# Kernel tuning notes

Hardware: AMD Instinct MI355X
Metric: run time of the kernel (lower is better)

## Reference

```python
import jax, jax.numpy as jnp
import numpy as np

H = 8  # num_heads

def setup_inputs() -> dict:
    key = jax.random.key(0)
    ks = jax.random.split(key, 8)
    N, B, E = 1024, 8, 256
    value = jax.random.normal(ks[0], (N, B, E), dtype=jnp.float32)
    pos = jax.random.normal(ks[1], (B * H, N, N), dtype=jnp.float32)
    s = 1.0 / np.sqrt(E)
    in_proj_w = jax.random.uniform(ks[2], (3 * E, E), jnp.float32, -s, s)   # content attn qkv proj
    in_proj_b = jnp.zeros((3 * E,), jnp.float32)
    out_w = jax.random.uniform(ks[3], (E, E), jnp.float32, -s, s)
    out_b = jnp.zeros((E,), jnp.float32)
    return {"value": value, "position_attention_weights": pos,
            "in_proj_w": in_proj_w, "in_proj_b": in_proj_b,
            "out_w": out_w, "out_b": out_b}

def reference(value, position_attention_weights, in_proj_w, in_proj_b, out_w, out_b):
    # value: (N, B, E) seq-first, position_attention_weights: (B*H, N, N)
    N, B, E = value.shape
    Dh = E // H
    qkv = value @ in_proj_w.T + in_proj_b            # (N, B, 3E)
    q, k, v = jnp.split(qkv, 3, axis=-1)
    # (N, B, E) -> (B*H, N, Dh)
    def to_heads(t):
        return t.reshape(N, B * H, Dh).transpose(1, 0, 2)
    q, k, v = to_heads(q), to_heads(k), to_heads(v)
    scale = 1.0 / jnp.sqrt(jnp.asarray(Dh, q.dtype))
    content = jnp.einsum('bnd,bmd->bnm', q * scale, k)   # (B*H, N, N) content scores
    # merge_attention == 'gate': clamp both, log-sigmoid gate on positional, add
    content = jnp.clip(content, -10.0, 10.0)
    pos = jnp.clip(position_attention_weights, -10.0, 10.0)
    scores = jax.nn.log_sigmoid(pos) + content
    attn = jax.nn.softmax(scores, axis=-1)               # normalizer
    out = jnp.einsum('bnm,bmd->bnd', attn, v)            # (B*H, N, Dh)
    out = out.transpose(1, 0, 2).reshape(N, B, E)        # back to (N, B, E)
    out = out @ out_w.T + out_b
    attn_avg = attn.reshape(B, H, N, N).mean(axis=1)     # averaged attention weights
    return out, attn_avg
```

## Files before the change

### kernel.cpp

```cpp
#include <hip/hip_runtime.h>
#include <hip/hip_bf16.h>

typedef __attribute__((ext_vector_type(8))) short short8;
typedef __attribute__((ext_vector_type(4))) float f32x4;
typedef __attribute__((ext_vector_type(4))) unsigned short u16x4;

#define MFMA16(a,b,c) __builtin_amdgcn_mfma_f32_16x16x32_bf16((a),(b),(c),0,0,0)

__device__ __forceinline__ ushort f2bf(float x) {
  union { float f; unsigned u; } v; v.f = x;
  unsigned u = v.u;
  u = (u + 0x7fffu + ((u >> 16) & 1u)) >> 16;
  return (ushort)u;
}

__device__ __forceinline__ float bf2f(ushort u) {
  union { unsigned u; float f; } v; v.u = ((unsigned)u) << 16;
  return v.f;
}

__device__ __forceinline__ short8 ld8(const ushort* p) {
  return *reinterpret_cast<const short8*>(p);
}

__global__ void conv_kernel(const float* __restrict__ value,
                            const float* __restrict__ w_in,
                            const float* __restrict__ w_out,
                            ushort* __restrict__ vbf,
                            ushort* __restrict__ wbf,
                            ushort* __restrict__ owbf) {
  int i = blockIdx.x * 256 + threadIdx.x;
  const float* src; ushort* dst; int j;
  if (i < 524288)      { src = value; dst = vbf;  j = i; }
  else if (i < 573440) { src = w_in;  dst = wbf;  j = i - 524288; }
  else                 { src = w_out; dst = owbf; j = i - 573440; }
  float4 v = reinterpret_cast<const float4*>(src)[j];
  u16x4 o;
  o[0] = f2bf(v.x); o[1] = f2bf(v.y); o[2] = f2bf(v.z); o[3] = f2bf(v.w);
  reinterpret_cast<u16x4*>(dst)[j] = o;
}

__global__ __launch_bounds__(256) void qkv_kernel(
    const ushort* __restrict__ vbf, const ushort* __restrict__ wbf,
    const float* __restrict__ bias,
    ushort* __restrict__ qh, ushort* __restrict__ kh, ushort* __restrict__ vv) {
  int tid = threadIdx.x;
  int wave = tid >> 6, lane = tid & 63;
  int lq = lane & 15, lg = lane >> 4;
  int r0 = blockIdx.x * 16;
  int c0 = (blockIdx.y * 4 + wave) * 16;
  f32x4 acc = {0.f, 0.f, 0.f, 0.f};
  const ushort* ap = vbf + (size_t)(r0 + lq) * 256 + lg * 8;
  const ushort* bp = wbf + (size_t)(c0 + lq) * 256 + lg * 8;
#pragma unroll
  for (int k0 = 0; k0 < 256; k0 += 32)
    acc = MFMA16(ld8(ap + k0), ld8(bp + k0), acc);
  int c = c0 + lq;
  float bv = bias[c];
#pragma unroll
  for (int r = 0; r < 4; ++r) {
    int row = r0 + lg * 4 + r;
    int n = row >> 3, b = row & 7;
    float v = acc[r] + bv;
    if (c < 256) {
      int h = c >> 5, d = c & 31;
      qh[((size_t)(b * 8 + h) * 1024 + n) * 32 + d] = f2bf(v * 0.17677669529663689f);
    } else if (c < 512) {
      int cc = c - 256, h = cc >> 5, d = cc & 31;
      kh[((size_t)(b * 8 + h) * 1024 + n) * 32 + d] = f2bf(v);
    } else {
      int cc = c - 512, h = cc >> 5, d = cc & 31;
      vv[((size_t)(b * 8 + h) * 1024 + n) * 32 + d] = f2bf(v);
    }
  }
}

__global__ __launch_bounds__(256) void vtrans_kernel(const ushort* __restrict__ vv,
                                                     ushort* __restrict__ vt) {
  __shared__ ushort t[32][73];
  int tid = threadIdx.x;
  int bh = blockIdx.y, m0 = blockIdx.x * 64;
  int mm = tid >> 2, d0 = (tid & 3) * 8;
  short8 v = ld8(vv + ((size_t)bh * 1024 + m0 + mm) * 32 + d0);
#pragma unroll
  for (int j = 0; j < 8; ++j) t[d0 + j][mm] = (ushort)v[j];
  __syncthreads();
  int d = tid >> 3, mg = (tid & 7) * 8;
  short8 o;
#pragma unroll
  for (int j = 0; j < 8; ++j) o[j] = (short)t[d][mg + j];
  *reinterpret_cast<short8*>(vt + ((size_t)bh * 32 + d) * 1024 + m0 + mg) = o;
}

__global__ __launch_bounds__(512, 4) void attn_kernel(
    const ushort* __restrict__ qh, const ushort* __restrict__ kh,
    const ushort* __restrict__ vt, const float* __restrict__ pos,
    ushort* __restrict__ ao, float* __restrict__ avg_out) {
  __shared__ __align__(16) ushort attn_lds[16][1028];
  __shared__ float pvred[8][16][32];
  __shared__ float rowsumT[16][8];

  int tid = threadIdx.x;
  int wave = tid >> 6, lane = tid & 63;
  int lq = lane & 15, lg = lane >> 4;
  int n0 = blockIdx.x * 16;
  int b = blockIdx.y;
  int mb = wave * 128;

  float avg[8][4];
#pragma unroll
  for (int t = 0; t < 8; ++t)
#pragma unroll
    for (int r = 0; r < 4; ++r) avg[t][r] = 0.f;

  for (int h = 0; h < 8; ++h) {
    int bh = b * 8 + h;
    short8 qa = ld8(qh + ((size_t)bh * 1024 + n0 + lq) * 32 + lg * 8);
    const ushort* kp = kh + (size_t)bh * 32768 + lg * 8;
    const float* pp = pos + ((size_t)bh << 20);
    float rs[4] = {0.f, 0.f, 0.f, 0.f};
    short8 wreg[4];

    {
      f32x4 S[4];
#pragma unroll
      for (int t = 0; t < 4; ++t) {
        f32x4 z = {0.f, 0.f, 0.f, 0.f};
        S[t] = MFMA16(qa, ld8(kp + (size_t)(mb + lq * 8 + t) * 32), z);
      }
#pragma unroll
      for (int r = 0; r < 4; ++r) {
        int n = n0 + lg * 4 + r;
        float4 p0 = *reinterpret_cast<const float4*>(pp + (size_t)n * 1024 + mb + lq * 8);
        float pv[4] = {p0.x, p0.y, p0.z, p0.w};
#pragma unroll
        for (int t = 0; t < 4; ++t) {
          float p = fminf(10.f, fmaxf(-10.f, pv[t]));
          float c = fminf(10.f, fmaxf(-10.f, S[t][r]));
          float w = __expf(c - 10.f) * __builtin_amdgcn_rcpf(1.f + __expf(-p));
          rs[r] += w;
          wreg[r][t] = (short)f2bf(w);
        }
      }
    }
    {
      f32x4 S[4];
#pragma unroll
      for (int t = 0; t < 4; ++t) {
        f32x4 z = {0.f, 0.f, 0.f, 0.f};
        S[t] = MFMA16(qa, ld8(kp + (size_t)(mb + lq * 8 + 4 + t) * 32), z);
      }
#pragma unroll
      for (int r = 0; r < 4; ++r) {
        int n = n0 + lg * 4 + r;
        float4 p1 = *reinterpret_cast<const float4*>(pp + (size_t)n * 1024 + mb + lq * 8 + 4);
        float pv[4] = {p1.x, p1.y, p1.z, p1.w};
#pragma unroll
        for (int t = 0; t < 4; ++t) {
          float p = fminf(10.f, fmaxf(-10.f, pv[t]));
          float c = fminf(10.f, fmaxf(-10.f, S[t][r]));
          float w = __expf(c - 10.f) * __builtin_amdgcn_rcpf(1.f + __expf(-p));
          rs[r] += w;
          wreg[r][4 + t] = (short)f2bf(w);
        }
      }
    }
#pragma unroll
    for (int r = 0; r < 4; ++r) {
      int row = lg * 4 + r;
      int col = (mb + lq * 8) ^ ((row & 7) << 3);
      *reinterpret_cast<short8*>(&attn_lds[row][col]) = wreg[r];
    }
#pragma unroll
    for (int r = 0; r < 4; ++r) {
      rs[r] += __shfl_xor(rs[r], 1);
      rs[r] += __shfl_xor(rs[r], 2);
      rs[r] += __shfl_xor(rs[r], 4);
      rs[r] += __shfl_xor(rs[r], 8);
    }
    if (lq == 0) {
#pragma unroll
      for (int r = 0; r < 4; ++r) rowsumT[lg * 4 + r][wave] = rs[r];
    }
    f32x4 acc0 = {0.f, 0.f, 0.f, 0.f}, acc1 = {0.f, 0.f, 0.f, 0.f};
    const ushort* vp = vt + (size_t)bh * 32768 + mb + lg * 8;
#pragma unroll
    for (int ks = 0; ks < 4; ++ks) {
      int col = (mb + ks * 32 + lg * 8) ^ ((lq & 7) << 3);
      short8 pa = *reinterpret_cast<const short8*>(&attn_lds[lq][col]);
      acc0 = MFMA16(pa, ld8(vp + (size_t)lq * 1024 + ks * 32), acc0);
      acc1 = MFMA16(pa, ld8(vp + (size_t)(lq + 16) * 1024 + ks * 32), acc1);
    }
    __syncthreads();
    float inv[4];
#pragma unroll
    for (int r = 0; r < 4; ++r) {
      int row = lg * 4 + r;
      float4 a0 = *reinterpret_cast<const float4*>(&rowsumT[row][0]);
      float4 a1 = *reinterpret_cast<const float4*>(&rowsumT[row][4]);
      inv[r] = __builtin_amdgcn_rcpf(a0.x + a0.y + a0.z + a0.w +
                                     a1.x + a1.y + a1.z + a1.w);
    }
#pragma unroll
    for (int r = 0; r < 4; ++r) {
      int row = lg * 4 + r;
      pvred[wave][row][lq] = acc0[r] * inv[r];
      pvred[wave][row][lq + 16] = acc1[r] * inv[r];
    }
#pragma unroll
    for (int r = 0; r < 4; ++r)
#pragma unroll
      for (int t = 0; t < 8; ++t)
        avg[t][r] += bf2f((ushort)wreg[r][t]) * inv[r];
    __syncthreads();
    {
      int n = tid >> 5, d = tid & 31;
      float s = 0.f;
#pragma unroll
      for (int w = 0; w < 8; ++w) s += pvred[w][n][d];
      ao[((size_t)(n0 + n) * 8 + b) * 256 + h * 32 + d] = f2bf(s);
    }
  }
#pragma unroll
  for (int r = 0; r < 4; ++r) {
    int n = n0 + lg * 4 + r;
    float* op = avg_out + (size_t)b * 1048576 + (size_t)n * 1024 + mb + lq * 8;
    float4 v0 = {avg[0][r] * 0.125f, avg[1][r] * 0.125f, avg[2][r] * 0.125f, avg[3][r] * 0.125f};
    float4 v1 = {avg[4][r] * 0.125f, avg[5][r] * 0.125f, avg[6][r] * 0.125f, avg[7][r] * 0.125f};
    *reinterpret_cast<float4*>(op) = v0;
    *reinterpret_cast<float4*>(op + 4) = v1;
  }
}

__global__ __launch_bounds__(256) void oproj_kernel(
    const ushort* __restrict__ ao, const ushort* __restrict__ owbf,
    const float* __restrict__ ob, float* __restrict__ outp) {
  int tid = threadIdx.x;
  int wave = tid >> 6, lane = tid & 63;
  int lq = lane & 15, lg = lane >> 4;
  int r0 = blockIdx.x * 16;
  int c0 = (blockIdx.y * 4 + wave) * 16;
  f32x4 acc = {0.f, 0.f, 0.f, 0.f};
  const ushort* ap = ao + (size_t)(r0 + lq) * 256 + lg * 8;
  const ushort* bp = owbf + (size_t)(c0 + lq) * 256 + lg * 8;
#pragma unroll
  for (int k0 = 0; k0 < 256; k0 += 32)
    acc = MFMA16(ld8(ap + k0), ld8(bp + k0), acc);
  int c = c0 + lq;
  float bv = ob[c];
#pragma unroll
  for (int r = 0; r < 4; ++r) {
    int row = r0 + lg * 4 + r;
    outp[(size_t)row * 256 + c] = acc[r] + bv;
  }
}

extern "C" void kernel_launch(void* const* d_in, const int* in_sizes, int n_in,
                              void* d_out, int out_size, void* d_ws, size_t ws_size,
                              hipStream_t stream) {
  const float* value = (const float*)d_in[0];
  const float* pos   = (const float*)d_in[1];
  const float* w_in  = (const float*)d_in[2];
  const float* b_in  = (const float*)d_in[3];
  const float* w_out = (const float*)d_in[4];
  const float* b_out = (const float*)d_in[5];

  char* ws = (char*)d_ws;
  ushort* vbf  = (ushort*)(ws);
  ushort* wbf  = (ushort*)(ws + 4194304);
  ushort* owbf = (ushort*)(ws + 4587520);
  ushort* qh   = (ushort*)(ws + 4718592);
  ushort* kh   = (ushort*)(ws + 8912896);
  ushort* vv   = (ushort*)(ws + 13107200);
  ushort* vt   = (ushort*)(ws);
  ushort* ao   = (ushort*)(ws + 17301504);

  float* outp = (float*)d_out;
  float* avgp = outp + 2097152;

  conv_kernel<<<2304, 256, 0, stream>>>(value, w_in, w_out, vbf, wbf, owbf);
  qkv_kernel<<<dim3(512, 12), 256, 0, stream>>>(vbf, wbf, b_in, qh, kh, vv);
  vtrans_kernel<<<dim3(16, 64), 256, 0, stream>>>(vv, vt);
  attn_kernel<<<dim3(64, 8), 512, 0, stream>>>(qh, kh, vt, pos, ao, avgp);
  oproj_kernel<<<dim3(512, 4), 256, 0, stream>>>(ao, owbf, b_out, outp);
}
```

Baseline: 181.8 us.

## Prefetch next head's positional tile, double-buffer reductions, drop one barrier per head

Loads the positional-weight tile for the next head during the current head's PV MFMAs and issues K loads early. The pvred and rowsum shared buffers are double-buffered so one of the two __syncthreads per head can go. Softmax normalisation moves into the post-barrier reduction. Non-temporal loads and stores are used for the streamed pos input and the averaged-attention output. This aims to hide HBM latency on the large pos stream, which dominates this memory-bound kernel, at the cost of more registers under launch_bounds(512,4).

```diff
diff --git a/kernel.cpp b/kernel.cpp
--- a/kernel.cpp
+++ b/kernel.cpp
@@ -21,6 +21,14 @@
 
 __device__ __forceinline__ short8 ld8(const ushort* p) {
   return *reinterpret_cast<const short8*>(p);
+}
+
+__device__ __forceinline__ f32x4 ldnt4(const float* p) {
+  return __builtin_nontemporal_load(reinterpret_cast<const f32x4*>(p));
+}
+
+__device__ __forceinline__ void stnt4(float* p, f32x4 v) {
+  __builtin_nontemporal_store(v, reinterpret_cast<f32x4*>(p));
 }
 
 __global__ void conv_kernel(const float* __restrict__ value,
@@ -97,8 +105,8 @@
     const ushort* __restrict__ vt, const float* __restrict__ pos,
     ushort* __restrict__ ao, float* __restrict__ avg_out) {
   __shared__ __align__(16) ushort attn_lds[16][1028];
-  __shared__ float pvred[8][16][32];
-  __shared__ float rowsumT[16][8];
+  __shared__ __align__(16) float pvred[2][8][16][32];
+  __shared__ __align__(16) float rowsumT[2][16][8];
 
   int tid = threadIdx.x;
   int wave = tid >> 6, lane = tid & 63;
@@ -113,29 +121,42 @@
 #pragma unroll
     for (int r = 0; r < 4; ++r) avg[t][r] = 0.f;
 
+  const float* prow0 = pos + ((size_t)(b * 8) << 20) + (size_t)(n0 + lg * 4) * 1024 + mb + lq * 8;
+
+  f32x4 pA[4];
+#pragma unroll
+  for (int r = 0; r < 4; ++r) pA[r] = ldnt4(prow0 + (size_t)r * 1024);
+
+  int buf = 0;
   for (int h = 0; h < 8; ++h) {
     int bh = b * 8 + h;
+    const float* prow = prow0 + ((size_t)h << 20);
+    const ushort* kp = kh + (size_t)bh * 32768 + lg * 8;
+
     short8 qa = ld8(qh + ((size_t)bh * 1024 + n0 + lq) * 32 + lg * 8);
-    const ushort* kp = kh + (size_t)bh * 32768 + lg * 8;
-    const float* pp = pos + ((size_t)bh << 20);
+    short8 ka0 = ld8(kp + (size_t)(mb + lq * 8 + 0) * 32);
+    short8 ka1 = ld8(kp + (size_t)(mb + lq * 8 + 1) * 32);
+    short8 ka2 = ld8(kp + (size_t)(mb + lq * 8 + 2) * 32);
+    short8 ka3 = ld8(kp + (size_t)(mb + lq * 8 + 3) * 32);
+    f32x4 pB[4];
+#pragma unroll
+    for (int r = 0; r < 4; ++r) pB[r] = ldnt4(prow + (size_t)r * 1024 + 4);
+
     float rs[4] = {0.f, 0.f, 0.f, 0.f};
     short8 wreg[4];
 
     {
-      f32x4 S[4];
-#pragma unroll
-      for (int t = 0; t < 4; ++t) {
-        f32x4 z = {0.f, 0.f, 0.f, 0.f};
-        S[t] = MFMA16(qa, ld8(kp + (size_t)(mb + lq * 8 + t) * 32), z);
-      }
+      f32x4 z = {0.f, 0.f, 0.f, 0.f};
+      f32x4 S0 = MFMA16(qa, ka0, z);
+      f32x4 S1 = MFMA16(qa, ka1, z);
+      f32x4 S2 = MFMA16(qa, ka2, z);
+      f32x4 S3 = MFMA16(qa, ka3, z);
+      f32x4 S[4] = {S0, S1, S2, S3};
 #pragma unroll
       for (int r = 0; r < 4; ++r) {
-        int n = n0 + lg * 4 + r;
-        float4 p0 = *reinterpret_cast<const float4*>(pp + (size_t)n * 1024 + mb + lq * 8);
-        float pv[4] = {p0.x, p0.y, p0.z, p0.w};
 #pragma unroll
         for (int t = 0; t < 4; ++t) {
-          float p = fminf(10.f, fmaxf(-10.f, pv[t]));
+          float p = fminf(10.f, fmaxf(-10.f, pA[r][t]));
           float c = fminf(10.f, fmaxf(-10.f, S[t][r]));
           float w = __expf(c - 10.f) * __builtin_amdgcn_rcpf(1.f + __expf(-p));
           rs[r] += w;
@@ -144,20 +165,21 @@
       }
     }
     {
-      f32x4 S[4];
-#pragma unroll
-      for (int t = 0; t < 4; ++t) {
-        f32x4 z = {0.f, 0.f, 0.f, 0.f};
-        S[t] = MFMA16(qa, ld8(kp + (size_t)(mb + lq * 8 + 4 + t) * 32), z);
-      }
+      short8 kb0 = ld8(kp + (size_t)(mb + lq * 8 + 4) * 32);
+      short8 kb1 = ld8(kp + (size_t)(mb + lq * 8 + 5) * 32);
+      short8 kb2 = ld8(kp + (size_t)(mb + lq * 8 + 6) * 32);
+      short8 kb3 = ld8(kp + (size_t)(mb + lq * 8 + 7) * 32);
+      f32x4 z = {0.f, 0.f, 0.f, 0.f};
+      f32x4 S0 = MFMA16(qa, kb0, z);
+      f32x4 S1 = MFMA16(qa, kb1, z);
+      f32x4 S2 = MFMA16(qa, kb2, z);
+      f32x4 S3 = MFMA16(qa, kb3, z);
+      f32x4 S[4] = {S0, S1, S2, S3};
 #pragma unroll
       for (int r = 0; r < 4; ++r) {
-        int n = n0 + lg * 4 + r;
-        float4 p1 = *reinterpret_cast<const float4*>(pp + (size_t)n * 1024 + mb + lq * 8 + 4);
-        float pv[4] = {p1.x, p1.y, p1.z, p1.w};
 #pragma unroll
         for (int t = 0; t < 4; ++t) {
-          float p = fminf(10.f, fmaxf(-10.f, pv[t]));
+          float p = fminf(10.f, fmaxf(-10.f, pB[r][t]));
           float c = fminf(10.f, fmaxf(-10.f, S[t][r]));
           float w = __expf(c - 10.f) * __builtin_amdgcn_rcpf(1.f + __expf(-p));
           rs[r] += w;
@@ -180,7 +202,7 @@
     }
     if (lq == 0) {
 #pragma unroll
-      for (int r = 0; r < 4; ++r) rowsumT[lg * 4 + r][wave] = rs[r];
+      for (int r = 0; r < 4; ++r) rowsumT[buf][lg * 4 + r][wave] = rs[r];
     }
     f32x4 acc0 = {0.f, 0.f, 0.f, 0.f}, acc1 = {0.f, 0.f, 0.f, 0.f};
     const ushort* vp = vt + (size_t)bh * 32768 + mb + lg * 8;
@@ -191,44 +213,49 @@
       acc0 = MFMA16(pa, ld8(vp + (size_t)lq * 1024 + ks * 32), acc0);
       acc1 = MFMA16(pa, ld8(vp + (size_t)(lq + 16) * 1024 + ks * 32), acc1);
     }
-    __syncthreads();
-    float inv[4];
+    if (h < 7) {
+      const float* pn = prow + (1u << 20);
+#pragma unroll
+      for (int r = 0; r < 4; ++r) pA[r] = ldnt4(pn + (size_t)r * 1024);
+    }
 #pragma unroll
     for (int r = 0; r < 4; ++r) {
-      int row = lg * 4 + r;
-      float4 a0 = *reinterpret_cast<const float4*>(&rowsumT[row][0]);
-      float4 a1 = *reinterpret_cast<const float4*>(&rowsumT[row][4]);
-      inv[r] = __builtin_amdgcn_rcpf(a0.x + a0.y + a0.z + a0.w +
-                                     a1.x + a1.y + a1.z + a1.w);
-    }
-#pragma unroll
-    for (int r = 0; r < 4; ++r) {
-      int row = lg * 4 + r;
-      pvred[wave][row][lq] = acc0[r] * inv[r];
-      pvred[wave][row][lq + 16] = acc1[r] * inv[r];
-    }
-#pragma unroll
-    for (int r = 0; r < 4; ++r)
-#pragma unroll
-      for (int t = 0; t < 8; ++t)
-        avg[t][r] += bf2f((ushort)wreg[r][t]) * inv[r];
+      pvred[buf][wave][lg * 4 + r][lq] = acc0[r];
+      pvred[buf][wave][lg * 4 + r][lq + 16] = acc1[r];
+    }
     __syncthreads();
     {
+#pragma unroll
+      for (int r = 0; r < 4; ++r) {
+        int row = lg * 4 + r;
+        float4 a0 = *reinterpret_cast<const float4*>(&rowsumT[buf][row][0]);
+        float4 a1 = *reinterpret_cast<const float4*>(&rowsumT[buf][row][4]);
+        float invr = __builtin_amdgcn_rcpf(a0.x + a0.y + a0.z + a0.w +
+                                           a1.x + a1.y + a1.z + a1.w);
+#pragma unroll
+        for (int t = 0; t < 8; ++t)
+          avg[t][r] += bf2f((ushort)wreg[r][t]) * invr;
+      }
       int n = tid >> 5, d = tid & 31;
+      float4 a0 = *reinterpret_cast<const float4*>(&rowsumT[buf][n][0]);
+      float4 a1 = *reinterpret_cast<const float4*>(&rowsumT[buf][n][4]);
+      float invn = __builtin_amdgcn_rcpf(a0.x + a0.y + a0.z + a0.w +
+                                         a1.x + a1.y + a1.z + a1.w);
       float s = 0.f;
 #pragma unroll
-      for (int w = 0; w < 8; ++w) s += pvred[w][n][d];
-      ao[((size_t)(n0 + n) * 8 + b) * 256 + h * 32 + d] = f2bf(s);
-    }
+      for (int w = 0; w < 8; ++w) s += pvred[buf][w][n][d];
+      ao[((size_t)(n0 + n) * 8 + b) * 256 + h * 32 + d] = f2bf(s * invn);
+    }
+    buf ^= 1;
   }
 #pragma unroll
   for (int r = 0; r < 4; ++r) {
     int n = n0 + lg * 4 + r;
     float* op = avg_out + (size_t)b * 1048576 + (size_t)n * 1024 + mb + lq * 8;
-    float4 v0 = {avg[0][r] * 0.125f, avg[1][r] * 0.125f, avg[2][r] * 0.125f, avg[3][r] * 0.125f};
-    float4 v1 = {avg[4][r] * 0.125f, avg[5][r] * 0.125f, avg[6][r] * 0.125f, avg[7][r] * 0.125f};
-    *reinterpret_cast<float4*>(op) = v0;
-    *reinterpret_cast<float4*>(op + 4) = v1;
+    f32x4 v0 = {avg[0][r] * 0.125f, avg[1][r] * 0.125f, avg[2][r] * 0.125f, avg[3][r] * 0.125f};
+    f32x4 v1 = {avg[4][r] * 0.125f, avg[5][r] * 0.125f, avg[6][r] * 0.125f, avg[7][r] * 0.125f};
+    stnt4(op, v0);
+    stnt4(op + 4, v1);
   }
 }
 
```

After: 213.3 us. 1.17x slower.

## Double-buffer positional scores into LDS via async global_load_lds in attention kernel

Applied to the files above, without the earlier changes.

The positional score tiles are now streamed into a double-buffered LDS array with global_load_lds, prefetching the next half-row chunk while the current one is processed. Each head is split into two halves, each with its own QK, weight and PV steps, and the column mapping per wave changes to suit. Softmax normalisation is deferred to the reduction step, which removes one barrier dependency, and the averaged-attention output uses nontemporal stores. This adds about 66KB of LDS, so launch bounds drop occupancy from 4 to 2 blocks, and there are more barriers per head.

```diff
diff --git a/kernel.cpp b/kernel.cpp
--- a/kernel.cpp
+++ b/kernel.cpp
@@ -21,6 +21,12 @@
 
 __device__ __forceinline__ short8 ld8(const ushort* p) {
   return *reinterpret_cast<const short8*>(p);
+}
+
+__device__ __forceinline__ void glds16(const float* g, float* l) {
+  __builtin_amdgcn_global_load_lds(
+      (const __attribute__((address_space(1))) unsigned int*)g,
+      (__attribute__((address_space(3))) unsigned int*)(void*)l, 16, 0, 0);
 }
 
 __global__ void conv_kernel(const float* __restrict__ value,
@@ -92,12 +98,13 @@
   *reinterpret_cast<short8*>(vt + ((size_t)bh * 32 + d) * 1024 + m0 + mg) = o;
 }
 
-__global__ __launch_bounds__(512, 4) void attn_kernel(
+__global__ __launch_bounds__(512, 2) void attn_kernel(
     const ushort* __restrict__ qh, const ushort* __restrict__ kh,
     const ushort* __restrict__ vt, const float* __restrict__ pos,
     ushort* __restrict__ ao, float* __restrict__ avg_out) {
-  __shared__ __align__(16) ushort attn_lds[16][1028];
-  __shared__ float pvred[8][16][32];
+  __shared__ __align__(16) float pos_lds[2][16][516];
+  __shared__ __align__(16) ushort attn_lds[16][1032];
+  __shared__ __align__(16) float pvred[8][16][32];
   __shared__ float rowsumT[16][8];
 
   int tid = threadIdx.x;
@@ -105,72 +112,77 @@
   int lq = lane & 15, lg = lane >> 4;
   int n0 = blockIdx.x * 16;
   int b = blockIdx.y;
-  int mb = wave * 128;
+
+  auto stage = [&](int s) {
+    int buf = s & 1;
+    const float* gb = pos + ((size_t)(b * 8 + (s >> 1)) << 20)
+                          + (size_t)n0 * 1024 + (s & 1) * 512;
+    int r = wave * 2;
+    glds16(gb + (size_t)r * 1024 +       lane * 4, &pos_lds[buf][r][0]);
+    glds16(gb + (size_t)r * 1024 + 256 + lane * 4, &pos_lds[buf][r][256]);
+    glds16(gb + (size_t)(r + 1) * 1024 +       lane * 4, &pos_lds[buf][r + 1][0]);
+    glds16(gb + (size_t)(r + 1) * 1024 + 256 + lane * 4, &pos_lds[buf][r + 1][256]);
+  };
 
   float avg[8][4];
 #pragma unroll
-  for (int t = 0; t < 8; ++t)
-#pragma unroll
-    for (int r = 0; r < 4; ++r) avg[t][r] = 0.f;
+  for (int j = 0; j < 8; ++j)
+#pragma unroll
+    for (int r = 0; r < 4; ++r) avg[j][r] = 0.f;
+
+  stage(0);
+  stage(1);
+  __syncthreads();
 
   for (int h = 0; h < 8; ++h) {
     int bh = b * 8 + h;
+    const ushort* kp = kh + (size_t)bh * 32768;
+    const ushort* vp = vt + (size_t)bh * 32768;
     short8 qa = ld8(qh + ((size_t)bh * 1024 + n0 + lq) * 32 + lg * 8);
-    const ushort* kp = kh + (size_t)bh * 32768 + lg * 8;
-    const float* pp = pos + ((size_t)bh << 20);
+    f32x4 acc0 = {0.f, 0.f, 0.f, 0.f}, acc1 = {0.f, 0.f, 0.f, 0.f};
     float rs[4] = {0.f, 0.f, 0.f, 0.f};
-    short8 wreg[4];
-
-    {
+    u16x4 wA[4], wB[4];
+
+    auto half_body = [&](int hf, u16x4* wv) {
+      int buf = (h * 2 + hf) & 1;
+      int mwin = hf * 512 + wave * 64;
+      int lcol = wave * 64 + lq * 4;
       f32x4 S[4];
 #pragma unroll
       for (int t = 0; t < 4; ++t) {
         f32x4 z = {0.f, 0.f, 0.f, 0.f};
-        S[t] = MFMA16(qa, ld8(kp + (size_t)(mb + lq * 8 + t) * 32), z);
+        S[t] = MFMA16(qa, ld8(kp + (size_t)(mwin + lq * 4 + t) * 32 + lg * 8), z);
       }
 #pragma unroll
       for (int r = 0; r < 4; ++r) {
-        int n = n0 + lg * 4 + r;
-        float4 p0 = *reinterpret_cast<const float4*>(pp + (size_t)n * 1024 + mb + lq * 8);
-        float pv[4] = {p0.x, p0.y, p0.z, p0.w};
+        int row = lg * 4 + r;
+        f32x4 pv = *reinterpret_cast<const f32x4*>(&pos_lds[buf][row][lcol]);
 #pragma unroll
         for (int t = 0; t < 4; ++t) {
           float p = fminf(10.f, fmaxf(-10.f, pv[t]));
           float c = fminf(10.f, fmaxf(-10.f, S[t][r]));
           float w = __expf(c - 10.f) * __builtin_amdgcn_rcpf(1.f + __expf(-p));
           rs[r] += w;
-          wreg[r][t] = (short)f2bf(w);
+          wv[r][t] = f2bf(w);
         }
+        int col = (mwin + lq * 4) ^ ((row & 7) << 3);
+        *reinterpret_cast<u16x4*>(&attn_lds[row][col]) = wv[r];
       }
-    }
-    {
-      f32x4 S[4];
-#pragma unroll
-      for (int t = 0; t < 4; ++t) {
-        f32x4 z = {0.f, 0.f, 0.f, 0.f};
-        S[t] = MFMA16(qa, ld8(kp + (size_t)(mb + lq * 8 + 4 + t) * 32), z);
+#pragma unroll
+      for (int ks = 0; ks < 2; ++ks) {
+        int sb = mwin + ks * 32;
+        int acol = (sb + lg * 8) ^ ((lq & 7) << 3);
+        short8 pa = *reinterpret_cast<const short8*>(&attn_lds[lq][acol]);
+        acc0 = MFMA16(pa, ld8(vp + (size_t)lq * 1024 + sb + lg * 8), acc0);
+        acc1 = MFMA16(pa, ld8(vp + (size_t)(lq + 16) * 1024 + sb + lg * 8), acc1);
       }
-#pragma unroll
-      for (int r = 0; r < 4; ++r) {
-        int n = n0 + lg * 4 + r;
-        float4 p1 = *reinterpret_cast<const float4*>(pp + (size_t)n * 1024 + mb + lq * 8 + 4);
-        float pv[4] = {p1.x, p1.y, p1.z, p1.w};
-#pragma unroll
-        for (int t = 0; t < 4; ++t) {
-          float p = fminf(10.f, fmaxf(-10.f, pv[t]));
-          float c = fminf(10.f, fmaxf(-10.f, S[t][r]));
-          float w = __expf(c - 10.f) * __builtin_amdgcn_rcpf(1.f + __expf(-p));
-          rs[r] += w;
-          wreg[r][4 + t] = (short)f2bf(w);
-        }
-      }
-    }
-#pragma unroll
-    for (int r = 0; r < 4; ++r) {
-      int row = lg * 4 + r;
-      int col = (mb + lq * 8) ^ ((row & 7) << 3);
-      *reinterpret_cast<short8*>(&attn_lds[row][col]) = wreg[r];
-    }
+    };
+
+    half_body(0, wA);
+    __syncthreads();
+    if (h * 2 + 2 < 16) stage(h * 2 + 2);
+    half_body(1, wB);
+
 #pragma unroll
     for (int r = 0; r < 4; ++r) {
       rs[r] += __shfl_xor(rs[r], 1);
@@ -182,53 +194,45 @@
 #pragma unroll
       for (int r = 0; r < 4; ++r) rowsumT[lg * 4 + r][wave] = rs[r];
     }
-    f32x4 acc0 = {0.f, 0.f, 0.f, 0.f}, acc1 = {0.f, 0.f, 0.f, 0.f};
-    const ushort* vp = vt + (size_t)bh * 32768 + mb + lg * 8;
-#pragma unroll
-    for (int ks = 0; ks < 4; ++ks) {
-      int col = (mb + ks * 32 + lg * 8) ^ ((lq & 7) << 3);
-      short8 pa = *reinterpret_cast<const short8*>(&attn_lds[lq][col]);
-      acc0 = MFMA16(pa, ld8(vp + (size_t)lq * 1024 + ks * 32), acc0);
-      acc1 = MFMA16(pa, ld8(vp + (size_t)(lq + 16) * 1024 + ks * 32), acc1);
+#pragma unroll
+    for (int r = 0; r < 4; ++r) {
+      pvred[wave][lg * 4 + r][lq] = acc0[r];
+      pvred[wave][lg * 4 + r][lq + 16] = acc1[r];
     }
     __syncthreads();
-    float inv[4];
+    if (h * 2 + 3 < 16) stage(h * 2 + 3);
 #pragma unroll
     for (int r = 0; r < 4; ++r) {
       int row = lg * 4 + r;
       float4 a0 = *reinterpret_cast<const float4*>(&rowsumT[row][0]);
       float4 a1 = *reinterpret_cast<const float4*>(&rowsumT[row][4]);
-      inv[r] = __builtin_amdgcn_rcpf(a0.x + a0.y + a0.z + a0.w +
-                                     a1.x + a1.y + a1.z + a1.w);
-    }
-#pragma unroll
-    for (int r = 0; r < 4; ++r) {
-      int row = lg * 4 + r;
-      pvred[wave][row][lq] = acc0[r] * inv[r];
-      pvred[wave][row][lq + 16] = acc1[r] * inv[r];
-    }
-#pragma unroll
-    for (int r = 0; r < 4; ++r)
-#pragma unroll
-      for (int t = 0; t < 8; ++t)
-        avg[t][r] += bf2f((ushort)wreg[r][t]) * inv[r];
-    __syncthreads();
+      float invr = __builtin_amdgcn_rcpf(a0.x + a0.y + a0.z + a0.w +
+                                         a1.x + a1.y + a1.z + a1.w);
+#pragma unroll
+      for (int j = 0; j < 4; ++j) avg[j][r] += bf2f(wA[r][j]) * invr;
+#pragma unroll
+      for (int j = 0; j < 4; ++j) avg[4 + j][r] += bf2f(wB[r][j]) * invr;
+    }
     {
       int n = tid >> 5, d = tid & 31;
+      float4 a0 = *reinterpret_cast<const float4*>(&rowsumT[n][0]);
+      float4 a1 = *reinterpret_cast<const float4*>(&rowsumT[n][4]);
+      float invn = __builtin_amdgcn_rcpf(a0.x + a0.y + a0.z + a0.w +
+                                         a1.x + a1.y + a1.z + a1.w);
       float s = 0.f;
 #pragma unroll
       for (int w = 0; w < 8; ++w) s += pvred[w][n][d];
-      ao[((size_t)(n0 + n) * 8 + b) * 256 + h * 32 + d] = f2bf(s);
+      ao[((size_t)(n0 + n) * 8 + b) * 256 + h * 32 + d] = f2bf(s * invn);
     }
   }
 #pragma unroll
   for (int r = 0; r < 4; ++r) {
     int n = n0 + lg * 4 + r;
-    float* op = avg_out + (size_t)b * 1048576 + (size_t)n * 1024 + mb + lq * 8;
-    float4 v0 = {avg[0][r] * 0.125f, avg[1][r] * 0.125f, avg[2][r] * 0.125f, avg[3][r] * 0.125f};
-    float4 v1 = {avg[4][r] * 0.125f, avg[5][r] * 0.125f, avg[6][r] * 0.125f, avg[7][r] * 0.125f};
-    *reinterpret_cast<float4*>(op) = v0;
-    *reinterpret_cast<float4*>(op + 4) = v1;
+    float* op = avg_out + (size_t)b * 1048576 + (size_t)n * 1024;
+    f32x4 v0 = {avg[0][r] * 0.125f, avg[1][r] * 0.125f, avg[2][r] * 0.125f, avg[3][r] * 0.125f};
+    f32x4 v1 = {avg[4][r] * 0.125f, avg[5][r] * 0.125f, avg[6][r] * 0.125f, avg[7][r] * 0.125f};
+    __builtin_nontemporal_store(v0, reinterpret_cast<f32x4*>(op + wave * 64 + lq * 4));
+    __builtin_nontemporal_store(v1, reinterpret_cast<f32x4*>(op + 512 + wave * 64 + lq * 4));
   }
 }
 
```

New measurement: 178.8 us. About the same (-1.6%).
